# Performance work log

Measured on AMD Instinct MI355X. Metric: run time of the kernel, lower is better.

## Reference

```python
import jax, jax.numpy as jnp
import numpy as np

B, N, H = 16, 128, 768
NEG = -1e9


def setup_inputs() -> dict:
    key = jax.random.key(0)
    ks = jax.random.split(key, 8)
    dec_outputs = jax.random.normal(ks[0], (B, N, H), jnp.float32)
    sen_vec = jax.random.normal(ks[1], (B, N, H), jnp.float32)
    Wq = jax.random.normal(ks[2], (H, H), jnp.float32) * 0.02
    bq = jnp.zeros((H,), jnp.float32)
    Wk = jax.random.normal(ks[3], (H, H), jnp.float32) * 0.02
    bk = jnp.zeros((H,), jnp.float32)
    wt = jax.random.normal(ks[4], (H,), jnp.float32) * 0.02
    bt = jnp.zeros((1,), jnp.float32)
    perm_keys = jax.random.split(ks[5], B)
    target = jax.vmap(lambda kk: jax.random.permutation(kk, N))(perm_keys).astype(jnp.int32)
    tgt_len = jax.random.randint(ks[6], (B,), 2, N + 1, dtype=jnp.int32)
    return dict(dec_outputs=dec_outputs, sen_vec=sen_vec, Wq=Wq, bq=bq, Wk=Wk,
                bk=bk, wt=wt, bt=bt, target=target, tgt_len=tgt_len)


def reference(dec_outputs, sen_vec, Wq, bq, Wk, bk, wt, bt, target, tgt_len):
    # query_linear / key_linear
    query = dec_outputs @ Wq + bq            # [B,T,H]
    key_ = sen_vec @ Wk + bk                 # [B,J,H]
    # pointer scores: tanh_linear(tanh(q_t + k_j))
    e = jnp.tanh(query[:, :, None, :] + key_[:, None, :, :])   # [B,T,J,H]
    scores = jnp.einsum('btjh,h->btj', e, wt) + bt[0]           # [B,T,J]

    # pointed_mask[b,t,j] = 1 iff j in target[b,:t]  (row t=0 all zeros)
    onehot = jax.nn.one_hot(target, N, dtype=scores.dtype)      # [B,T,N]
    cum = jnp.cumsum(onehot, axis=1)
    pointed = jnp.concatenate([jnp.zeros_like(cum[:, :1]), cum[:, :-1]], axis=1) > 0

    valid = jnp.arange(N)[None, :] < tgt_len[:, None]            # [B,N] col/row validity
    lens = tgt_len.astype(scores.dtype)

    # --- row loss: masked log-softmax over columns + NLL(reduction='none') ---
    e_row = jnp.where(pointed, NEG, scores)
    e_row = jnp.where(valid[:, None, :], e_row, NEG)
    logp = jax.nn.log_softmax(e_row, axis=-1)                    # [B,T,J]
    nll = -jnp.take_along_axis(logp, target[..., None], axis=-1)[..., 0]  # [B,T]
    nll = jnp.where(valid, nll, 0.0)                             # target_mask == valid (square)
    row_loss = jnp.mean(jnp.sum(nll, axis=-1) / (lens + 1e-20 - 1.0))

    # --- column loss: log-softmax over rows (dim=1), NLL against arange labels ---
    e_col = jnp.where(valid[:, None, :], scores, NEG)            # mask invalid columns
    e_col = jnp.where(valid[:, :, None], e_col, NEG)             # mask invalid rows
    logp2 = jax.nn.log_softmax(e_col, axis=1)                    # softmax over t
    nll2 = -jnp.take_along_axis(logp2, target[..., None], axis=-1)[..., 0]  # [B,T]
    nll2 = jnp.where(valid, nll2, 0.0)
    # per-batch: NLLLoss mean over len, then / (len - 1 + eps)
    col_loss = jnp.mean(jnp.sum(nll2, axis=-1) / (lens * (lens + 1e-20 - 1.0)))

    return row_loss + col_loss
```

## Files before the change

kernel.cpp:

```cpp
#include <hip/hip_runtime.h>
#include <math.h>

#define B_ 16
#define N_ 128
#define H_ 768
#define NEGV (-1e9f)
#define CFAC 2.8853900817779268f

typedef float f32x4 __attribute__((ext_vector_type(4)));
typedef short s16x8 __attribute__((ext_vector_type(8)));
typedef short s16x4 __attribute__((ext_vector_type(4)));

__device__ __forceinline__ unsigned short f2bf(float x) {
    unsigned int u = __float_as_uint(x);
    u += 0x7fffu + ((u >> 16) & 1u);
    return (unsigned short)(u >> 16);
}
__device__ __forceinline__ float bf2f(unsigned short h) {
    return __uint_as_float(((unsigned int)h) << 16);
}

__device__ __forceinline__ float wave_sum(float v) {
    #pragma unroll
    for (int o = 32; o > 0; o >>= 1) v += __shfl_down(v, o);
    return v;
}
__device__ __forceinline__ float wave_max(float v) {
    #pragma unroll
    for (int o = 32; o > 0; o >>= 1) v = fmaxf(v, __shfl_down(v, o));
    return v;
}

__global__ __launch_bounds__(256) void gemm_kernel(const float* __restrict__ dec,
                                                   const float* __restrict__ sen,
                                                   const float* __restrict__ Wq,
                                                   const float* __restrict__ bq,
                                                   const float* __restrict__ Wk,
                                                   const float* __restrict__ bk,
                                                   const float* __restrict__ wt,
                                                   const int* __restrict__ target,
                                                   const int* __restrict__ tgt_len,
                                                   float* __restrict__ eq,
                                                   float* __restrict__ ek,
                                                   int* __restrict__ inv,
                                                   float* __restrict__ w2,
                                                   float* __restrict__ sumwt) {
    const int tid = threadIdx.x;

    if (blockIdx.z == 2) {
        if (blockIdx.y != 0) return;
        const int p = blockIdx.x;
        if (p < B_) {
            if (tid < N_) inv[p * N_ + target[p * N_ + tid]] = tid;
        } else if (p == B_) {
            __shared__ float red[4];
            float local = 0.f;
            for (int h = tid; h < H_; h += 256) {
                float w = wt[h];
                w2[h] = -2.f * w;
                local += w;
            }
            float v = wave_sum(local);
            if ((tid & 63) == 0) red[tid >> 6] = v;
            __syncthreads();
            if (tid == 0) sumwt[0] = red[0] + red[1] + red[2] + red[3];
        }
        return;
    }

    const float* A; const float* W; const float* bias; float* out;
    if (blockIdx.z == 0) { A = dec; W = Wq; bias = bq; out = eq; }
    else                 { A = sen; W = Wk; bias = bk; out = ek; }

    const int bx = blockIdx.x;
    const int m0 = bx * 64;
    if (((bx & 1) * 64) >= tgt_len[bx >> 1]) return;
    const int n0 = blockIdx.y * 128;

    const int lane = tid & 63;
    const int wid  = tid >> 6;
    const int wr = wid >> 1, wc = wid & 1;
    const int l15 = lane & 15, lhi = lane >> 4;

    __shared__ unsigned short Ah[64 * 40], Al[64 * 40];
    __shared__ unsigned short Bh[128 * 40], Bl[128 * 40];

    f32x4 acc[2][4];
    #pragma unroll
    for (int fm = 0; fm < 2; fm++)
        #pragma unroll
        for (int fn = 0; fn < 4; fn++) acc[fm][fn] = (f32x4){0.f, 0.f, 0.f, 0.f};

    const int arow = tid >> 2;
    const int akc  = (tid & 3) * 8;
    const int bk4  = tid >> 5;
    const int bnc  = (tid & 31) * 4;

    for (int k0 = 0; k0 < H_; k0 += 32) {
        const float* ap = &A[(m0 + arow) * H_ + k0 + akc];
        float4 a0 = *(const float4*)ap;
        float4 a1 = *(const float4*)(ap + 4);
        const float* wp = &W[(k0 + bk4 * 4) * H_ + n0 + bnc];
        float4 r0 = *(const float4*)wp;
        float4 r1 = *(const float4*)(wp + H_);
        float4 r2 = *(const float4*)(wp + 2 * H_);
        float4 r3 = *(const float4*)(wp + 3 * H_);

        __syncthreads();
        {
            float av[8] = {a0.x, a0.y, a0.z, a0.w, a1.x, a1.y, a1.z, a1.w};
            s16x8 hv, lv;
            #pragma unroll
            for (int i = 0; i < 8; i++) {
                unsigned short h = f2bf(av[i]);
                hv[i] = (short)h;
                lv[i] = (short)f2bf(av[i] - bf2f(h));
            }
            *(s16x8*)&Ah[arow * 40 + akc] = hv;
            *(s16x8*)&Al[arow * 40 + akc] = lv;
        }
        {
            float bm[4][4] = {{r0.x, r0.y, r0.z, r0.w},
                              {r1.x, r1.y, r1.z, r1.w},
                              {r2.x, r2.y, r2.z, r2.w},
                              {r3.x, r3.y, r3.z, r3.w}};
            #pragma unroll
            for (int j = 0; j < 4; j++) {
                s16x4 bh, bl;
                #pragma unroll
                for (int i = 0; i < 4; i++) {
                    unsigned short h = f2bf(bm[i][j]);
                    bh[i] = (short)h;
                    bl[i] = (short)f2bf(bm[i][j] - bf2f(h));
                }
                *(s16x4*)&Bh[(bnc + j) * 40 + bk4 * 4] = bh;
                *(s16x4*)&Bl[(bnc + j) * 40 + bk4 * 4] = bl;
            }
        }
        __syncthreads();

        s16x8 ahf[2], alf[2], bhf[4], blf[4];
        #pragma unroll
        for (int fm = 0; fm < 2; fm++) {
            int off = (wr * 32 + fm * 16 + l15) * 40 + lhi * 8;
            ahf[fm] = *(const s16x8*)&Ah[off];
            alf[fm] = *(const s16x8*)&Al[off];
        }
        #pragma unroll
        for (int fn = 0; fn < 4; fn++) {
            int off = (wc * 64 + fn * 16 + l15) * 40 + lhi * 8;
            bhf[fn] = *(const s16x8*)&Bh[off];
            blf[fn] = *(const s16x8*)&Bl[off];
        }
        #pragma unroll
        for (int fm = 0; fm < 2; fm++)
            #pragma unroll
            for (int fn = 0; fn < 4; fn++) {
                acc[fm][fn] = __builtin_amdgcn_mfma_f32_16x16x32_bf16(alf[fm], bhf[fn], acc[fm][fn], 0, 0, 0);
                acc[fm][fn] = __builtin_amdgcn_mfma_f32_16x16x32_bf16(ahf[fm], blf[fn], acc[fm][fn], 0, 0, 0);
                acc[fm][fn] = __builtin_amdgcn_mfma_f32_16x16x32_bf16(ahf[fm], bhf[fn], acc[fm][fn], 0, 0, 0);
            }
    }

    #pragma unroll
    for (int fm = 0; fm < 2; fm++)
        #pragma unroll
        for (int fn = 0; fn < 4; fn++) {
            int col = n0 + wc * 64 + fn * 16 + l15;
            float bv = bias[col];
            #pragma unroll
            for (int r = 0; r < 4; r++) {
                int row = m0 + wr * 32 + fm * 16 + lhi * 4 + r;
                out[row * H_ + col] = __builtin_amdgcn_exp2f(CFAC * (acc[fm][fn][r] + bv));
            }
        }
}

__global__ __launch_bounds__(512) void scores_kernel(const float* __restrict__ eq,
                                                     const float* __restrict__ ek,
                                                     const float* __restrict__ w2,
                                                     const float* __restrict__ sumwt,
                                                     const float* __restrict__ bt,
                                                     const int* __restrict__ tgt_len,
                                                     float* __restrict__ sc) {
    const int b  = blockIdx.z;
    const int t0 = blockIdx.y * 8;
    const int j0 = blockIdx.x * 64;
    const int len = tgt_len[b];
    if (t0 >= len || j0 >= len) return;

    const int tid  = threadIdx.x;
    const int lane = tid & 63;
    const int wv   = tid >> 6;

    __shared__ __align__(16) float ks[64][128];
    __shared__ __align__(16) float qs[8][128];
    __shared__ __align__(16) float w2s[H_];

    for (int h = tid; h < H_; h += 512) w2s[h] = w2[h];

    const int krow = tid >> 3;
    const int kcg  = (tid & 7) * 16;
    const bool doq = tid < 256;
    const int qrow = (tid >> 5) & 7;
    const int qcol = (tid & 31) * 4;

    const float* kbase = &ek[(b * N_ + j0 + krow) * H_ + kcg];
    const float* qbase = &eq[(b * N_ + t0 + qrow) * H_ + qcol];

    float4 kf[4]; float4 qf;
    #pragma unroll
    for (int i = 0; i < 4; i++) kf[i] = *(const float4*)&kbase[4 * i];
    if (doq) qf = *(const float4*)&qbase[0];

    const int kswz = (krow & 7) << 2;
    const int rswz = (lane & 7) << 2;
    float acc = 0.f;

    for (int h0 = 0; h0 < H_; h0 += 128) {
        __syncthreads();
        #pragma unroll
        for (int i = 0; i < 4; i++)
            *(float4*)&ks[krow][(kcg + 4 * i) ^ kswz] = kf[i];
        if (doq) *(float4*)&qs[qrow][qcol] = qf;
        __syncthreads();
        if (h0 + 128 < H_) {
            #pragma unroll
            for (int i = 0; i < 4; i++) kf[i] = *(const float4*)&kbase[h0 + 128 + 4 * i];
            if (doq) qf = *(const float4*)&qbase[h0 + 128];
        }
        #pragma unroll
        for (int hh = 0; hh < 128; hh += 4) {
            float4 k4 = *(const float4*)&ks[lane][hh ^ rswz];
            float4 w4 = *(const float4*)&w2s[h0 + hh];
            float4 q4 = *(const float4*)&qs[wv][hh];
            acc = fmaf(w4.x, __builtin_amdgcn_rcpf(fmaf(q4.x, k4.x, 1.f)), acc);
            acc = fmaf(w4.y, __builtin_amdgcn_rcpf(fmaf(q4.y, k4.y, 1.f)), acc);
            acc = fmaf(w4.z, __builtin_amdgcn_rcpf(fmaf(q4.z, k4.z, 1.f)), acc);
            acc = fmaf(w4.w, __builtin_amdgcn_rcpf(fmaf(q4.w, k4.w, 1.f)), acc);
        }
    }

    sc[(b * N_ + t0 + wv) * N_ + j0 + lane] = acc + sumwt[0] + bt[0];
}

__global__ __launch_bounds__(128) void loss_kernel(const float* __restrict__ sc,
                                                   const int* __restrict__ inv,
                                                   const int* __restrict__ target,
                                                   const int* __restrict__ tgt_len,
                                                   float* __restrict__ rowterm,
                                                   float* __restrict__ colterm) {
    const int b = blockIdx.y;
    const int len = tgt_len[b];
    __shared__ float es[128];
    __shared__ float red[2];

    if (blockIdx.z == 0) {
        const int t = blockIdx.x, j = threadIdx.x;
        float s = sc[(b * N_ + t) * N_ + j];
        int invj = inv[b * N_ + j];
        float e = (invj < t || j >= len) ? NEGV : s;
        es[j] = e;
        float v = wave_max(e);
        if ((j & 63) == 0) red[j >> 6] = v;
        __syncthreads();
        float m = fmaxf(red[0], red[1]);
        __syncthreads();
        float p = __expf(e - m);
        float ps = wave_sum(p);
        if ((j & 63) == 0) red[j >> 6] = ps;
        __syncthreads();
        if (j == 0) {
            float sum = red[0] + red[1];
            int jt = target[b * N_ + t];
            float shifted = es[jt] - m;
            rowterm[b * N_ + t] = (t < len) ? (__logf(sum) - shifted) : 0.f;
        }
    } else {
        const int j = blockIdx.x, t = threadIdx.x;
        float s = sc[(b * N_ + t) * N_ + j];
        float e = (t < len && j < len) ? s : NEGV;
        es[t] = e;
        float v = wave_max(e);
        if ((t & 63) == 0) red[t >> 6] = v;
        __syncthreads();
        float m = fmaxf(red[0], red[1]);
        __syncthreads();
        float p = __expf(e - m);
        float ps = wave_sum(p);
        if ((t & 63) == 0) red[t >> 6] = ps;
        __syncthreads();
        if (t == 0) {
            float sum = red[0] + red[1];
            int ts = inv[b * N_ + j];
            float shifted = es[ts] - m;
            colterm[b * N_ + ts] = (ts < len) ? (__logf(sum) - shifted) : 0.f;
        }
    }
}

__global__ __launch_bounds__(128) void final_kernel(const float* __restrict__ rowterm,
                                                    const float* __restrict__ colterm,
                                                    const int* __restrict__ tgt_len,
                                                    float* __restrict__ out) {
    const int tid = threadIdx.x;
    __shared__ float red[2];
    float rowacc = 0.f, colacc = 0.f;
    for (int b = 0; b < B_; b++) {
        float r = rowterm[b * N_ + tid];
        float c = colterm[b * N_ + tid];
        float v = wave_sum(r);
        if ((tid & 63) == 0) red[tid >> 6] = v;
        __syncthreads();
        float rs = red[0] + red[1];
        __syncthreads();
        float w = wave_sum(c);
        if ((tid & 63) == 0) red[tid >> 6] = w;
        __syncthreads();
        float cs = red[0] + red[1];
        __syncthreads();
        if (tid == 0) {
            float lenf = (float)tgt_len[b];
            rowacc += rs / (lenf - 1.f);
            colacc += cs / (lenf * (lenf - 1.f));
        }
    }
    if (tid == 0) out[0] = rowacc / (float)B_ + colacc / (float)B_;
}

extern "C" void kernel_launch(void* const* d_in, const int* in_sizes, int n_in,
                              void* d_out, int out_size, void* d_ws, size_t ws_size,
                              hipStream_t stream) {
    (void)in_sizes; (void)n_in; (void)out_size; (void)ws_size;
    const float* dec = (const float*)d_in[0];
    const float* sen = (const float*)d_in[1];
    const float* Wq  = (const float*)d_in[2];
    const float* bq  = (const float*)d_in[3];
    const float* Wk  = (const float*)d_in[4];
    const float* bk  = (const float*)d_in[5];
    const float* wt  = (const float*)d_in[6];
    const float* bt  = (const float*)d_in[7];
    const int* target  = (const int*)d_in[8];
    const int* tgt_len = (const int*)d_in[9];

    float* ws = (float*)d_ws;
    float* eq      = ws;
    float* ek      = ws + 1572864;
    float* sc      = ws + 3145728;
    int*   inv     = (int*)(ws + 3407872);
    float* w2      = ws + 3409920;
    float* sumwt   = ws + 3410688;
    float* rowterm = ws + 3410692;
    float* colterm = ws + 3412740;
    float* out = (float*)d_out;

    gemm_kernel<<<dim3(32, 6, 3), 256, 0, stream>>>(dec, sen, Wq, bq, Wk, bk, wt,
                                                    target, tgt_len, eq, ek, inv, w2, sumwt);
    scores_kernel<<<dim3(2, 16, 16), 512, 0, stream>>>(eq, ek, w2, sumwt, bt, tgt_len, sc);
    loss_kernel<<<dim3(N_, B_, 2), 128, 0, stream>>>(sc, inv, target, tgt_len, rowterm, colterm);
    final_kernel<<<1, 128, 0, stream>>>(rowterm, colterm, tgt_len, out);
}
```

Baseline: 179.0 us.

## Pre-pack weights to bf16 fragments, drop split-bf16 GEMM, store exp activations as bf16

Adds a prep kernel that converts Wq/Wk to bf16 once per call, already laid out as MFMA B-fragments. The GEMM becomes LDS-free: each wave streams its A rows from global, converts them to bf16 and issues a single MFMA per fragment instead of three hi/lo split products. The exponentiated query/key outputs are stored as bf16, which halves their write and read traffic in the scores kernel. This trades fp32-like accuracy of the projection and exp values for less compute and bandwidth, which risks tolerance failures, and it adds an extra kernel launch.

New measurement: 160.6 us. 1.11x faster.

```diff
diff --git a/kernel.cpp b/kernel.cpp
--- a/kernel.cpp
+++ b/kernel.cpp
@@ -31,59 +31,89 @@
     return v;
 }
 
-__global__ __launch_bounds__(256) void gemm_kernel(const float* __restrict__ dec,
-                                                   const float* __restrict__ sen,
-                                                   const float* __restrict__ Wq,
-                                                   const float* __restrict__ bq,
+__global__ __launch_bounds__(128) void prep_kernel(const float* __restrict__ Wq,
                                                    const float* __restrict__ Wk,
-                                                   const float* __restrict__ bk,
                                                    const float* __restrict__ wt,
                                                    const int* __restrict__ target,
-                                                   const int* __restrict__ tgt_len,
-                                                   float* __restrict__ eq,
-                                                   float* __restrict__ ek,
+                                                   unsigned short* __restrict__ wqbf,
+                                                   unsigned short* __restrict__ wkbf,
                                                    int* __restrict__ inv,
                                                    float* __restrict__ w2,
                                                    float* __restrict__ sumwt) {
+    const int bid = blockIdx.x;
     const int tid = threadIdx.x;
-
-    if (blockIdx.z == 2) {
-        if (blockIdx.y != 0) return;
-        const int p = blockIdx.x;
-        if (p < B_) {
-            if (tid < N_) inv[p * N_ + target[p * N_ + tid]] = tid;
-        } else if (p == B_) {
-            __shared__ float red[4];
-            float local = 0.f;
-            for (int h = tid; h < H_; h += 256) {
-                float w = wt[h];
-                w2[h] = -2.f * w;
-                local += w;
-            }
-            float v = wave_sum(local);
-            if ((tid & 63) == 0) red[tid >> 6] = v;
-            __syncthreads();
-            if (tid == 0) sumwt[0] = red[0] + red[1] + red[2] + red[3];
-        }
-        return;
-    }
-
-    const float* A; const float* W; const float* bias; float* out;
-    if (blockIdx.z == 0) { A = dec; W = Wq; bias = bq; out = eq; }
-    else                 { A = sen; W = Wk; bias = bk; out = ek; }
-
-    const int bx = blockIdx.x;
-    const int m0 = bx * 64;
-    if (((bx & 1) * 64) >= tgt_len[bx >> 1]) return;
-    const int n0 = blockIdx.y * 128;
-
-    const int lane = tid & 63;
-    const int wid  = tid >> 6;
-    const int wr = wid >> 1, wc = wid & 1;
+    if (bid < 576) {
+        const float* W = (bid < 288) ? Wq : Wk;
+        unsigned short* dst = (bid < 288) ? wqbf : wkbf;
+        const int tb = bid % 288;
+        const int kg = tb % 24, nt = tb / 24;
+        const int k0 = kg * 32, n0 = nt * 64;
+
+        __shared__ float tile[32][68];
+        const int tr = tid >> 2, tc = (tid & 3) * 16;
+        const float* src = &W[(k0 + tr) * H_ + n0 + tc];
+        float4 v0 = *(const float4*)(src);
+        float4 v1 = *(const float4*)(src + 4);
+        float4 v2 = *(const float4*)(src + 8);
+        float4 v3 = *(const float4*)(src + 12);
+        *(float4*)&tile[tr][tc]      = v0;
+        *(float4*)&tile[tr][tc + 4]  = v1;
+        *(float4*)&tile[tr][tc + 8]  = v2;
+        *(float4*)&tile[tr][tc + 12] = v3;
+        __syncthreads();
+
+        #pragma unroll
+        for (int c = 0; c < 2; c++) {
+            const int ch = tid + c * 128;
+            const int lane = ch & 63, ngl = ch >> 6;
+            const int nl = ngl * 16 + (lane & 15);
+            const int kl = (lane >> 4) * 8;
+            s16x8 o;
+            #pragma unroll
+            for (int i = 0; i < 8; i++) o[i] = (short)f2bf(tile[kl + i][nl]);
+            const int ng = nt * 4 + ngl;
+            *(s16x8*)&dst[((ng * 24 + kg) * 64 + lane) * 8] = o;
+        }
+    } else if (bid == 576) {
+        for (int i = tid; i < B_ * N_; i += 128) {
+            int b = i >> 7, t = i & 127;
+            inv[b * N_ + target[b * N_ + t]] = t;
+        }
+        __shared__ float red[2];
+        float local = 0.f;
+        for (int h = tid; h < H_; h += 128) {
+            float w = wt[h];
+            w2[h] = -2.f * w;
+            local += w;
+        }
+        float v = wave_sum(local);
+        if ((tid & 63) == 0) red[tid >> 6] = v;
+        __syncthreads();
+        if (tid == 0) sumwt[0] = red[0] + red[1];
+    }
+}
+
+__global__ __launch_bounds__(256) void gemm_kernel(const float* __restrict__ dec,
+                                                   const float* __restrict__ sen,
+                                                   const unsigned short* __restrict__ wqbf,
+                                                   const unsigned short* __restrict__ wkbf,
+                                                   const float* __restrict__ bq,
+                                                   const float* __restrict__ bk,
+                                                   const int* __restrict__ tgt_len,
+                                                   unsigned short* __restrict__ eqbf,
+                                                   unsigned short* __restrict__ ekbf) {
+    const int z = blockIdx.y;
+    const float* A = z ? sen : dec;
+    const unsigned short* Wb = z ? wkbf : wqbf;
+    const float* bias = z ? bk : bq;
+    unsigned short* out = z ? ekbf : eqbf;
+
+    const int tid = threadIdx.x, lane = tid & 63, w = tid >> 6;
+    const int wg = blockIdx.x * 4 + w;
+    const int mi = wg / 12, ni = wg - mi * 12;
+    const int m0 = mi * 32, n0 = ni * 64;
+    if ((m0 & 127) >= tgt_len[m0 >> 7]) return;
     const int l15 = lane & 15, lhi = lane >> 4;
-
-    __shared__ unsigned short Ah[64 * 40], Al[64 * 40];
-    __shared__ unsigned short Bh[128 * 40], Bl[128 * 40];
 
     f32x4 acc[2][4];
     #pragma unroll
@@ -91,93 +121,56 @@
         #pragma unroll
         for (int fn = 0; fn < 4; fn++) acc[fm][fn] = (f32x4){0.f, 0.f, 0.f, 0.f};
 
-    const int arow = tid >> 2;
-    const int akc  = (tid & 3) * 8;
-    const int bk4  = tid >> 5;
-    const int bnc  = (tid & 31) * 4;
-
-    for (int k0 = 0; k0 < H_; k0 += 32) {
-        const float* ap = &A[(m0 + arow) * H_ + k0 + akc];
-        float4 a0 = *(const float4*)ap;
-        float4 a1 = *(const float4*)(ap + 4);
-        const float* wp = &W[(k0 + bk4 * 4) * H_ + n0 + bnc];
-        float4 r0 = *(const float4*)wp;
-        float4 r1 = *(const float4*)(wp + H_);
-        float4 r2 = *(const float4*)(wp + 2 * H_);
-        float4 r3 = *(const float4*)(wp + 3 * H_);
-
-        __syncthreads();
-        {
-            float av[8] = {a0.x, a0.y, a0.z, a0.w, a1.x, a1.y, a1.z, a1.w};
-            s16x8 hv, lv;
-            #pragma unroll
-            for (int i = 0; i < 8; i++) {
-                unsigned short h = f2bf(av[i]);
-                hv[i] = (short)h;
-                lv[i] = (short)f2bf(av[i] - bf2f(h));
-            }
-            *(s16x8*)&Ah[arow * 40 + akc] = hv;
-            *(s16x8*)&Al[arow * 40 + akc] = lv;
-        }
-        {
-            float bm[4][4] = {{r0.x, r0.y, r0.z, r0.w},
-                              {r1.x, r1.y, r1.z, r1.w},
-                              {r2.x, r2.y, r2.z, r2.w},
-                              {r3.x, r3.y, r3.z, r3.w}};
-            #pragma unroll
-            for (int j = 0; j < 4; j++) {
-                s16x4 bh, bl;
-                #pragma unroll
-                for (int i = 0; i < 4; i++) {
-                    unsigned short h = f2bf(bm[i][j]);
-                    bh[i] = (short)h;
-                    bl[i] = (short)f2bf(bm[i][j] - bf2f(h));
-                }
-                *(s16x4*)&Bh[(bnc + j) * 40 + bk4 * 4] = bh;
-                *(s16x4*)&Bl[(bnc + j) * 40 + bk4 * 4] = bl;
-            }
-        }
-        __syncthreads();
-
-        s16x8 ahf[2], alf[2], bhf[4], blf[4];
-        #pragma unroll
-        for (int fm = 0; fm < 2; fm++) {
-            int off = (wr * 32 + fm * 16 + l15) * 40 + lhi * 8;
-            ahf[fm] = *(const s16x8*)&Ah[off];
-            alf[fm] = *(const s16x8*)&Al[off];
-        }
-        #pragma unroll
-        for (int fn = 0; fn < 4; fn++) {
-            int off = (wc * 64 + fn * 16 + l15) * 40 + lhi * 8;
-            bhf[fn] = *(const s16x8*)&Bh[off];
-            blf[fn] = *(const s16x8*)&Bl[off];
-        }
-        #pragma unroll
-        for (int fm = 0; fm < 2; fm++)
-            #pragma unroll
-            for (int fn = 0; fn < 4; fn++) {
-                acc[fm][fn] = __builtin_amdgcn_mfma_f32_16x16x32_bf16(alf[fm], bhf[fn], acc[fm][fn], 0, 0, 0);
-                acc[fm][fn] = __builtin_amdgcn_mfma_f32_16x16x32_bf16(ahf[fm], blf[fn], acc[fm][fn], 0, 0, 0);
-                acc[fm][fn] = __builtin_amdgcn_mfma_f32_16x16x32_bf16(ahf[fm], bhf[fn], acc[fm][fn], 0, 0, 0);
-            }
+    const float* aptr0 = &A[(m0 + l15) * H_ + lhi * 8];
+    const float* aptr1 = &A[(m0 + 16 + l15) * H_ + lhi * 8];
+    const unsigned short* bb = &Wb[((n0 >> 4) * 24) * 512 + lane * 8];
+
+    #pragma unroll 2
+    for (int kg = 0; kg < 24; kg++) {
+        s16x8 bf0 = *(const s16x8*)&bb[(0 * 24 + kg) * 512];
+        s16x8 bf1 = *(const s16x8*)&bb[(1 * 24 + kg) * 512];
+        s16x8 bf2 = *(const s16x8*)&bb[(2 * 24 + kg) * 512];
+        s16x8 bf3 = *(const s16x8*)&bb[(3 * 24 + kg) * 512];
+        float4 a00 = *(const float4*)(aptr0 + kg * 32);
+        float4 a01 = *(const float4*)(aptr0 + kg * 32 + 4);
+        float4 a10 = *(const float4*)(aptr1 + kg * 32);
+        float4 a11 = *(const float4*)(aptr1 + kg * 32 + 4);
+        s16x8 af0, af1;
+        af0[0] = (short)f2bf(a00.x); af0[1] = (short)f2bf(a00.y);
+        af0[2] = (short)f2bf(a00.z); af0[3] = (short)f2bf(a00.w);
+        af0[4] = (short)f2bf(a01.x); af0[5] = (short)f2bf(a01.y);
+        af0[6] = (short)f2bf(a01.z); af0[7] = (short)f2bf(a01.w);
+        af1[0] = (short)f2bf(a10.x); af1[1] = (short)f2bf(a10.y);
+        af1[2] = (short)f2bf(a10.z); af1[3] = (short)f2bf(a10.w);
+        af1[4] = (short)f2bf(a11.x); af1[5] = (short)f2bf(a11.y);
+        af1[6] = (short)f2bf(a11.z); af1[7] = (short)f2bf(a11.w);
+        acc[0][0] = __builtin_amdgcn_mfma_f32_16x16x32_bf16(af0, bf0, acc[0][0], 0, 0, 0);
+        acc[0][1] = __builtin_amdgcn_mfma_f32_16x16x32_bf16(af0, bf1, acc[0][1], 0, 0, 0);
+        acc[0][2] = __builtin_amdgcn_mfma_f32_16x16x32_bf16(af0, bf2, acc[0][2], 0, 0, 0);
+        acc[0][3] = __builtin_amdgcn_mfma_f32_16x16x32_bf16(af0, bf3, acc[0][3], 0, 0, 0);
+        acc[1][0] = __builtin_amdgcn_mfma_f32_16x16x32_bf16(af1, bf0, acc[1][0], 0, 0, 0);
+        acc[1][1] = __builtin_amdgcn_mfma_f32_16x16x32_bf16(af1, bf1, acc[1][1], 0, 0, 0);
+        acc[1][2] = __builtin_amdgcn_mfma_f32_16x16x32_bf16(af1, bf2, acc[1][2], 0, 0, 0);
+        acc[1][3] = __builtin_amdgcn_mfma_f32_16x16x32_bf16(af1, bf3, acc[1][3], 0, 0, 0);
     }
 
     #pragma unroll
     for (int fm = 0; fm < 2; fm++)
         #pragma unroll
         for (int fn = 0; fn < 4; fn++) {
-            int col = n0 + wc * 64 + fn * 16 + l15;
+            int col = n0 + fn * 16 + l15;
             float bv = bias[col];
             #pragma unroll
             for (int r = 0; r < 4; r++) {
-                int row = m0 + wr * 32 + fm * 16 + lhi * 4 + r;
-                out[row * H_ + col] = __builtin_amdgcn_exp2f(CFAC * (acc[fm][fn][r] + bv));
+                int row = m0 + fm * 16 + lhi * 4 + r;
+                out[row * H_ + col] =
+                    f2bf(__builtin_amdgcn_exp2f(CFAC * (acc[fm][fn][r] + bv)));
             }
         }
 }
 
-__global__ __launch_bounds__(512) void scores_kernel(const float* __restrict__ eq,
-                                                     const float* __restrict__ ek,
+__global__ __launch_bounds__(512) void scores_kernel(const unsigned short* __restrict__ eqbf,
+                                                     const unsigned short* __restrict__ ekbf,
                                                      const float* __restrict__ w2,
                                                      const float* __restrict__ sumwt,
                                                      const float* __restrict__ bt,
@@ -205,13 +198,13 @@
     const int qrow = (tid >> 5) & 7;
     const int qcol = (tid & 31) * 4;
 
-    const float* kbase = &ek[(b * N_ + j0 + krow) * H_ + kcg];
-    const float* qbase = &eq[(b * N_ + t0 + qrow) * H_ + qcol];
-
-    float4 kf[4]; float4 qf;
-    #pragma unroll
-    for (int i = 0; i < 4; i++) kf[i] = *(const float4*)&kbase[4 * i];
-    if (doq) qf = *(const float4*)&qbase[0];
+    const unsigned short* kr = &ekbf[(b * N_ + j0 + krow) * H_ + kcg];
+    const unsigned short* qb = &eqbf[(b * N_ + t0 + qrow) * H_ + qcol];
+
+    s16x8 kf0 = *(const s16x8*)&kr[0];
+    s16x8 kf1 = *(const s16x8*)&kr[8];
+    s16x4 qf;
+    if (doq) qf = *(const s16x4*)&qb[0];
 
     const int kswz = (krow & 7) << 2;
     const int rswz = (lane & 7) << 2;
@@ -220,14 +213,27 @@
     for (int h0 = 0; h0 < H_; h0 += 128) {
         __syncthreads();
         #pragma unroll
-        for (int i = 0; i < 4; i++)
-            *(float4*)&ks[krow][(kcg + 4 * i) ^ kswz] = kf[i];
-        if (doq) *(float4*)&qs[qrow][qcol] = qf;
+        for (int i = 0; i < 4; i++) {
+            float4 t;
+            t.x = bf2f((unsigned short)kf0[0]);
+            const int e = i * 4;
+            t.x = bf2f((unsigned short)((e + 0 < 8) ? kf0[(e + 0) & 7] : kf1[(e + 0) & 7]));
+            t.y = bf2f((unsigned short)((e + 1 < 8) ? kf0[(e + 1) & 7] : kf1[(e + 1) & 7]));
+            t.z = bf2f((unsigned short)((e + 2 < 8) ? kf0[(e + 2) & 7] : kf1[(e + 2) & 7]));
+            t.w = bf2f((unsigned short)((e + 3 < 8) ? kf0[(e + 3) & 7] : kf1[(e + 3) & 7]));
+            *(float4*)&ks[krow][(kcg + e) ^ kswz] = t;
+        }
+        if (doq) {
+            float4 t;
+            t.x = bf2f((unsigned short)qf[0]); t.y = bf2f((unsigned short)qf[1]);
+            t.z = bf2f((unsigned short)qf[2]); t.w = bf2f((unsigned short)qf[3]);
+            *(float4*)&qs[qrow][qcol] = t;
+        }
         __syncthreads();
         if (h0 + 128 < H_) {
-            #pragma unroll
-            for (int i = 0; i < 4; i++) kf[i] = *(const float4*)&kbase[h0 + 128 + 4 * i];
-            if (doq) qf = *(const float4*)&qbase[h0 + 128];
+            kf0 = *(const s16x8*)&kr[h0 + 128];
+            kf1 = *(const s16x8*)&kr[h0 + 136];
+            if (doq) qf = *(const s16x4*)&qb[h0 + 128];
         }
         #pragma unroll
         for (int hh = 0; hh < 128; hh += 4) {
@@ -344,19 +350,21 @@
     const int* tgt_len = (const int*)d_in[9];
 
     float* ws = (float*)d_ws;
-    float* eq      = ws;
-    float* ek      = ws + 1572864;
-    float* sc      = ws + 3145728;
-    int*   inv     = (int*)(ws + 3407872);
-    float* w2      = ws + 3409920;
-    float* sumwt   = ws + 3410688;
-    float* rowterm = ws + 3410692;
-    float* colterm = ws + 3412740;
+    unsigned short* eqbf = (unsigned short*)ws;
+    unsigned short* ekbf = (unsigned short*)(ws + 786432);
+    float* sc      = ws + 1572864;
+    int*   inv     = (int*)(ws + 1835008);
+    float* w2      = ws + 1837056;
+    float* sumwt   = ws + 1837824;
+    float* rowterm = ws + 1837828;
+    float* colterm = ws + 1839876;
+    unsigned short* wqbf = (unsigned short*)(ws + 1841924);
+    unsigned short* wkbf = (unsigned short*)(ws + 2136836);
     float* out = (float*)d_out;
 
-    gemm_kernel<<<dim3(32, 6, 3), 256, 0, stream>>>(dec, sen, Wq, bq, Wk, bk, wt,
-                                                    target, tgt_len, eq, ek, inv, w2, sumwt);
-    scores_kernel<<<dim3(2, 16, 16), 512, 0, stream>>>(eq, ek, w2, sumwt, bt, tgt_len, sc);
+    prep_kernel<<<dim3(577), 128, 0, stream>>>(Wq, Wk, wt, target, wqbf, wkbf, inv, w2, sumwt);
+    gemm_kernel<<<dim3(192, 2), 256, 0, stream>>>(dec, sen, wqbf, wkbf, bq, bk, tgt_len, eqbf, ekbf);
+    scores_kernel<<<dim3(2, 16, 16), 512, 0, stream>>>(eqbf, ekbf, w2, sumwt, bt, tgt_len, sc);
     loss_kernel<<<dim3(N_, B_, 2), 128, 0, stream>>>(sc, inv, target, tgt_len, rowterm, colterm);
     final_kernel<<<1, 128, 0, stream>>>(rowterm, colterm, tgt_len, out);
 }
```
